# Kernel tuning notes

Hardware: AMD Instinct MI355X
Metric: run time of the kernel (lower is better)

The kernel has to match this reference:

```python
import jax, jax.numpy as jnp
import numpy as np

B, E, N, D = 2048, 32, 32, 64  # batch, n_entities, n_neighbors, dim


def setup_inputs() -> dict:
    key = jax.random.key(0)
    k1, k2, k3, k4, k5 = jax.random.split(key, 5)
    return {
        "self_vectors": jax.random.normal(k1, (B, E, D), dtype=jnp.float32),
        "neighbor_vectors": jax.random.normal(k2, (B, E, N, D), dtype=jnp.float32),
        "neighbor_relations": jax.random.normal(k3, (B, E, N, D), dtype=jnp.float32),
        "user_embeddings": jax.random.normal(k4, (B, D), dtype=jnp.float32),
        "masks": jnp.ones((B, E), dtype=bool),  # unused by the module
        "W": jax.random.normal(k5, (D, D), dtype=jnp.float32) * (1.0 / np.sqrt(D)),
        "b_lin": jnp.zeros((D,), dtype=jnp.float32),
    }


def reference(self_vectors, neighbor_vectors, neighbor_relations, user_embeddings, masks, W, b_lin):
    # user-relation scores: mean over dim of (user [b,1,1,d] * relations [b,e,n,d])
    scores = jnp.einsum('bd,bend->ben', user_embeddings, neighbor_relations) / neighbor_relations.shape[-1]
    attn = jax.nn.softmax(scores, axis=-1)[..., None]          # [b,e,n,1]
    # torch.mean over neighbor axis of attn * neighbor_vectors
    neighbors_agg = jnp.mean(attn * neighbor_vectors, axis=2)  # [b,e,d]
    out = self_vectors + neighbors_agg                         # [b,e,d]
    out = out @ W.T + b_lin                                    # Linear (dropout p=0 -> identity)
    return jax.nn.relu(out)
```

## Files before the change

### kernel.cpp

```cpp
#include <hip/hip_runtime.h>

#define B_  2048
#define E_  32
#define N_  32
#define D_  64

__global__ __launch_bounds__(256) void kgcn_kernel(
    const float* __restrict__ self_v,
    const float* __restrict__ nv,
    const float* __restrict__ rel,
    const float* __restrict__ user,
    const float* __restrict__ W,
    const float* __restrict__ blin,
    float* __restrict__ out)
{
    const int be = blockIdx.x;
    const int b  = be >> 5;
    const int t  = threadIdx.x;
    const int n0 = t >> 4;
    const int d4 = t & 15;

    __shared__ float  s_score[N_];
    __shared__ float  s_attn[N_];
    __shared__ float4 s_acc[256];
    __shared__ float4 s_pre[D_ / 4];

    const float4* rel4 = (const float4*)rel + (size_t)be * 512;
    const float4* nv4  = (const float4*)nv  + (size_t)be * 512;

    float4 r0 = rel4[t];
    float4 r1 = rel4[t + 256];
    float4 v0 = nv4[t];
    float4 v1 = nv4[t + 256];
    float4 u4 = ((const float4*)user)[b * 16 + d4];

    float p0 = r0.x * u4.x + r0.y * u4.y + r0.z * u4.z + r0.w * u4.w;
    float p1 = r1.x * u4.x + r1.y * u4.y + r1.z * u4.z + r1.w * u4.w;

    #pragma unroll
    for (int m = 1; m < 16; m <<= 1) {
        p0 += __shfl_xor(p0, m);
        p1 += __shfl_xor(p1, m);
    }
    if (d4 == 0) {
        s_score[n0]      = p0 * (1.0f / (float)D_);
        s_score[n0 + 16] = p1 * (1.0f / (float)D_);
    }
    __syncthreads();

    if (t < N_) {
        float m = -1e30f;
        #pragma unroll
        for (int n = 0; n < N_; ++n) m = fmaxf(m, s_score[n]);
        float e = __expf(s_score[t] - m);
        s_attn[t] = e;
    }
    __syncthreads();
    if (t < N_) {
        float s = 0.0f;
        #pragma unroll
        for (int n = 0; n < N_; ++n) s += s_attn[n];
        s_score[t] = s_attn[t] / (s * (float)N_);
    }
    __syncthreads();

    {
        const float a0 = s_score[n0];
        const float a1 = s_score[n0 + 16];
        float4 acc;
        acc.x = a0 * v0.x + a1 * v1.x;
        acc.y = a0 * v0.y + a1 * v1.y;
        acc.z = a0 * v0.z + a1 * v1.z;
        acc.w = a0 * v0.w + a1 * v1.w;
        s_acc[t] = acc;
    }
    __syncthreads();

    if (t < 16) {
        float4 s = s_acc[t];
        #pragma unroll
        for (int k = 1; k < 16; ++k) {
            float4 x = s_acc[t + 16 * k];
            s.x += x.x; s.y += x.y; s.z += x.z; s.w += x.w;
        }
        float4 sv = ((const float4*)self_v)[(size_t)be * 16 + t];
        s.x += sv.x; s.y += sv.y; s.z += sv.z; s.w += sv.w;
        s_pre[t] = s;
    }
    __syncthreads();

    if (t < D_) {
        float acc = blin[t];
        const float4* Wrow = (const float4*)W + t * 16;
        #pragma unroll
        for (int k4 = 0; k4 < 16; ++k4) {
            float4 w = Wrow[k4];
            float4 p = s_pre[k4];
            acc += w.x * p.x + w.y * p.y + w.z * p.z + w.w * p.w;
        }
        out[(size_t)be * 64 + t] = fmaxf(acc, 0.0f);
    }
}

extern "C" void kernel_launch(void* const* d_in, const int* in_sizes, int n_in,
                              void* d_out, int out_size, void* d_ws, size_t ws_size,
                              hipStream_t stream) {
    const float* self_v = (const float*)d_in[0];
    const float* nv     = (const float*)d_in[1];
    const float* rel    = (const float*)d_in[2];
    const float* user   = (const float*)d_in[3];
    const float* W      = (const float*)d_in[5];
    const float* blin   = (const float*)d_in[6];
    float* out          = (float*)d_out;

    const int blocks = B_ * E_;
    kgcn_kernel<<<blocks, 256, 0, stream>>>(self_v, nv, rel, user, W, blin, out);
}
```

Measured before the change: 1.010 ms.

## Map one (batch, entity) pair per wavefront and drop shared-memory barriers

Each wavefront now handles a whole (b,e) pair. Every lane loads 8 float4 of relations and neighbors and does the softmax and weighted sum entirely with cross-lane shuffles, with no shared memory and no __syncthreads. The final linear layer broadcasts the pre-activation vector through readlane instead of LDS. This removes the several block-wide barriers and idle threads that the serial softmax had in the old one-block-per-pair design. The cost is higher register pressure from the 16 float4 loads per lane, which may limit occupancy of this memory-bound kernel.

```diff
diff --git a/kernel.cpp b/kernel.cpp
--- a/kernel.cpp
+++ b/kernel.cpp
@@ -5,7 +5,11 @@
 #define N_  32
 #define D_  64
 
-__global__ __launch_bounds__(256) void kgcn_kernel(
+__device__ __forceinline__ float readlane_f(float x, int l) {
+    return __int_as_float(__builtin_amdgcn_readlane(__float_as_int(x), l));
+}
+
+__global__ __launch_bounds__(256) void kgcn_wave_kernel(
     const float* __restrict__ self_v,
     const float* __restrict__ nv,
     const float* __restrict__ rel,
@@ -14,92 +18,81 @@
     const float* __restrict__ blin,
     float* __restrict__ out)
 {
-    const int be = blockIdx.x;
-    const int b  = be >> 5;
-    const int t  = threadIdx.x;
-    const int n0 = t >> 4;
-    const int d4 = t & 15;
-
-    __shared__ float  s_score[N_];
-    __shared__ float  s_attn[N_];
-    __shared__ float4 s_acc[256];
-    __shared__ float4 s_pre[D_ / 4];
+    const int t    = threadIdx.x;
+    const int wave = t >> 6;
+    const int lane = t & 63;
+    const int be   = blockIdx.x * 4 + wave;
+    const int b    = be >> 5;
+    const int d4   = lane & 15;
 
     const float4* rel4 = (const float4*)rel + (size_t)be * 512;
     const float4* nv4  = (const float4*)nv  + (size_t)be * 512;
 
-    float4 r0 = rel4[t];
-    float4 r1 = rel4[t + 256];
-    float4 v0 = nv4[t];
-    float4 v1 = nv4[t + 256];
+    float4 r[8], v[8];
+    #pragma unroll
+    for (int j = 0; j < 8; ++j) r[j] = rel4[lane + 64 * j];
+    #pragma unroll
+    for (int j = 0; j < 8; ++j) v[j] = nv4[lane + 64 * j];
     float4 u4 = ((const float4*)user)[b * 16 + d4];
+    float4 sv = ((const float4*)self_v)[(size_t)be * 16 + d4];
 
-    float p0 = r0.x * u4.x + r0.y * u4.y + r0.z * u4.z + r0.w * u4.w;
-    float p1 = r1.x * u4.x + r1.y * u4.y + r1.z * u4.z + r1.w * u4.w;
+    float s[8];
+    #pragma unroll
+    for (int j = 0; j < 8; ++j) {
+        float p = r[j].x * u4.x + r[j].y * u4.y + r[j].z * u4.z + r[j].w * u4.w;
+        p += __shfl_xor(p, 1);
+        p += __shfl_xor(p, 2);
+        p += __shfl_xor(p, 4);
+        p += __shfl_xor(p, 8);
+        s[j] = p * (1.0f / 64.0f);
+    }
 
+    float m = s[0];
     #pragma unroll
-    for (int m = 1; m < 16; m <<= 1) {
-        p0 += __shfl_xor(p0, m);
-        p1 += __shfl_xor(p1, m);
+    for (int j = 1; j < 8; ++j) m = fmaxf(m, s[j]);
+    m = fmaxf(m, __shfl_xor(m, 16));
+    m = fmaxf(m, __shfl_xor(m, 32));
+
+    float e[8];
+    float S = 0.0f;
+    #pragma unroll
+    for (int j = 0; j < 8; ++j) { e[j] = __expf(s[j] - m); S += e[j]; }
+    S += __shfl_xor(S, 16);
+    S += __shfl_xor(S, 32);
+    const float inv = 1.0f / (S * (float)N_);
+
+    float4 acc = {0.0f, 0.0f, 0.0f, 0.0f};
+    #pragma unroll
+    for (int j = 0; j < 8; ++j) {
+        const float a = e[j] * inv;
+        acc.x += a * v[j].x;
+        acc.y += a * v[j].y;
+        acc.z += a * v[j].z;
+        acc.w += a * v[j].w;
     }
-    if (d4 == 0) {
-        s_score[n0]      = p0 * (1.0f / (float)D_);
-        s_score[n0 + 16] = p1 * (1.0f / (float)D_);
+    acc.x += __shfl_xor(acc.x, 16);
+    acc.y += __shfl_xor(acc.y, 16);
+    acc.z += __shfl_xor(acc.z, 16);
+    acc.w += __shfl_xor(acc.w, 16);
+    acc.x += __shfl_xor(acc.x, 32);
+    acc.y += __shfl_xor(acc.y, 32);
+    acc.z += __shfl_xor(acc.z, 32);
+    acc.w += __shfl_xor(acc.w, 32);
+
+    acc.x += sv.x; acc.y += sv.y; acc.z += sv.z; acc.w += sv.w;
+
+    float o = blin[lane];
+    const float4* Wr = (const float4*)W + lane * 16;
+    #pragma unroll
+    for (int k4 = 0; k4 < 16; ++k4) {
+        float4 w = Wr[k4];
+        const float px = readlane_f(acc.x, k4);
+        const float py = readlane_f(acc.y, k4);
+        const float pz = readlane_f(acc.z, k4);
+        const float pw = readlane_f(acc.w, k4);
+        o += w.x * px + w.y * py + w.z * pz + w.w * pw;
     }
-    __syncthreads();
-
-    if (t < N_) {
-        float m = -1e30f;
-        #pragma unroll
-        for (int n = 0; n < N_; ++n) m = fmaxf(m, s_score[n]);
-        float e = __expf(s_score[t] - m);
-        s_attn[t] = e;
-    }
-    __syncthreads();
-    if (t < N_) {
-        float s = 0.0f;
-        #pragma unroll
-        for (int n = 0; n < N_; ++n) s += s_attn[n];
-        s_score[t] = s_attn[t] / (s * (float)N_);
-    }
-    __syncthreads();
-
-    {
-        const float a0 = s_score[n0];
-        const float a1 = s_score[n0 + 16];
-        float4 acc;
-        acc.x = a0 * v0.x + a1 * v1.x;
-        acc.y = a0 * v0.y + a1 * v1.y;
-        acc.z = a0 * v0.z + a1 * v1.z;
-        acc.w = a0 * v0.w + a1 * v1.w;
-        s_acc[t] = acc;
-    }
-    __syncthreads();
-
-    if (t < 16) {
-        float4 s = s_acc[t];
-        #pragma unroll
-        for (int k = 1; k < 16; ++k) {
-            float4 x = s_acc[t + 16 * k];
-            s.x += x.x; s.y += x.y; s.z += x.z; s.w += x.w;
-        }
-        float4 sv = ((const float4*)self_v)[(size_t)be * 16 + t];
-        s.x += sv.x; s.y += sv.y; s.z += sv.z; s.w += sv.w;
-        s_pre[t] = s;
-    }
-    __syncthreads();
-
-    if (t < D_) {
-        float acc = blin[t];
-        const float4* Wrow = (const float4*)W + t * 16;
-        #pragma unroll
-        for (int k4 = 0; k4 < 16; ++k4) {
-            float4 w = Wrow[k4];
-            float4 p = s_pre[k4];
-            acc += w.x * p.x + w.y * p.y + w.z * p.z + w.w * p.w;
-        }
-        out[(size_t)be * 64 + t] = fmaxf(acc, 0.0f);
-    }
+    out[(size_t)be * 64 + lane] = fmaxf(o, 0.0f);
 }
 
 extern "C" void kernel_launch(void* const* d_in, const int* in_sizes, int n_in,
@@ -113,6 +106,6 @@
     const float* blin   = (const float*)d_in[6];
     float* out          = (float*)d_out;
 
-    const int blocks = B_ * E_;
-    kgcn_kernel<<<blocks, 256, 0, stream>>>(self_v, nv, rel, user, W, blin, out);
+    const int blocks = (B_ * E_) / 4;
+    kgcn_wave_kernel<<<blocks, 256, 0, stream>>>(self_v, nv, rel, user, W, blin, out);
 }
```

New measurement: 1.020 ms. No clear change (+1.1%).
